# Performance work log

Measured on AMD Instinct MI355X. Metric: run time of the kernel, lower is better.

Reference implementation:

```python
import jax, jax.numpy as jnp
import numpy as np

NB_HEAD = 8
SIZE_PER_HEAD = 64
MAX_LEN = 1024
MASK_PENALTY = 1e12


def setup_inputs() -> dict:
    key = jax.random.key(0)
    ks = jax.random.split(key, 6)
    B, L, D_IN = 8, MAX_LEN, 512
    D_OUT = NB_HEAD * SIZE_PER_HEAD
    return {
        "Q_seq": jax.random.normal(ks[0], (B, L, D_IN), dtype=jnp.float32),
        "K_seq": jax.random.normal(ks[1], (B, L, D_IN), dtype=jnp.float32),
        "V_seq": jax.random.normal(ks[2], (B, L, D_IN), dtype=jnp.float32),
        "WQ": jax.random.normal(ks[3], (D_IN, D_OUT), dtype=jnp.float32) * 0.03,
        "WK": jax.random.normal(ks[4], (D_IN, D_OUT), dtype=jnp.float32) * 0.03,
        "WV": jax.random.normal(ks[5], (D_IN, D_OUT), dtype=jnp.float32) * 0.03,
    }


def reference(Q_seq, K_seq, V_seq, WQ, WK, WV):
    B, L, _ = Q_seq.shape
    H, D = NB_HEAD, SIZE_PER_HEAD
    # project and split heads: [B, L, H*D] -> [B, H, L, D]
    q = (Q_seq @ WQ).reshape(B, L, H, D).transpose(0, 2, 1, 3)
    k = (K_seq @ WK).reshape(B, L, H, D).transpose(0, 2, 1, 3)
    v = (V_seq @ WV).reshape(B, L, H, D).transpose(0, 2, 1, 3)
    scale = 1.0 / jnp.sqrt(jnp.asarray(D, dtype=q.dtype))
    scores = jnp.einsum('bhqd,bhkd->bhqk', q, k) * scale  # [B,H,L,L]
    # Mask(): eye+cumsum construction == causal mask (penalize key > query)
    causal = jnp.triu(jnp.ones((L, L), dtype=scores.dtype), k=1)
    scores = scores - causal * MASK_PENALTY
    A = jax.nn.softmax(scores, axis=-1)
    O = jnp.einsum('bhqk,bhkd->bhqd', A, v)  # [B,H,L,D]
    return O.transpose(0, 2, 1, 3).reshape(B, L, H * D)
```

## Files before the change

kernel.cpp:

```cpp
#include <hip/hip_runtime.h>

#define NH 8
#define DH 64
#define SL 1024
#define NB 8
#define DIN 512
#define DOUT 512
#define PS 72

typedef __bf16 bf16x8 __attribute__((ext_vector_type(8)));
typedef float floatx4 __attribute__((ext_vector_type(4)));
typedef unsigned short ushortx8 __attribute__((ext_vector_type(8)));

__device__ __forceinline__ unsigned short f2bf(float f) {
    unsigned int u = __builtin_bit_cast(unsigned int, f);
    u += 0x7FFFu + ((u >> 16) & 1u);
    return (unsigned short)(u >> 16);
}

__device__ __forceinline__ floatx4 mfma_bf16(bf16x8 a, bf16x8 b, floatx4 c) {
    return __builtin_amdgcn_mfma_f32_16x16x32_bf16(a, b, c, 0, 0, 0);
}

__device__ __forceinline__ void gld_lds16(const unsigned short* g, unsigned short* l) {
    __builtin_amdgcn_global_load_lds(
        (const __attribute__((address_space(1))) unsigned int*)g,
        (__attribute__((address_space(3))) unsigned int*)l, 16, 0, 0);
}

__device__ __forceinline__ unsigned int pack_bf2(float a, float b) {
    return __builtin_amdgcn_perm(__builtin_bit_cast(unsigned int, b),
                                 __builtin_bit_cast(unsigned int, a), 0x07060302u);
}

__global__ __launch_bounds__(256) void xbf_kernel(const float* __restrict__ Qs,
                                                  const float* __restrict__ Ks,
                                                  const float* __restrict__ Vs,
                                                  unsigned short* __restrict__ xb) {
    const int z = blockIdx.y;
    const float* X = (z == 0) ? Qs : (z == 1 ? Ks : Vs);
    const int t = blockIdx.x * 256 + threadIdx.x;
    const int row = t >> 6, c = t & 63;
    const float4 a = *(const float4*)(X + t * 8);
    const float4 b = *(const float4*)(X + t * 8 + 4);
    ushortx8 o;
    o[0] = f2bf(a.x); o[1] = f2bf(a.y); o[2] = f2bf(a.z); o[3] = f2bf(a.w);
    o[4] = f2bf(b.x); o[5] = f2bf(b.y); o[6] = f2bf(b.z); o[7] = f2bf(b.w);
    const int dst = (((row >> 7) * 8 + (c >> 3)) * 128 + (row & 127)) * 64 +
                    (((c & 7) ^ (row & 7)) * 8);
    *(ushortx8*)(xb + z * 8192 * DIN + dst) = o;
}

__global__ __launch_bounds__(256) void wt_kernel(const float* __restrict__ WQ,
                                                 const float* __restrict__ WK,
                                                 const float* __restrict__ WV,
                                                 unsigned short* __restrict__ wt) {
    __shared__ unsigned short tile[64][68];
    const int z = blockIdx.z;
    const float* W = (z == 0) ? WQ : (z == 1 ? WK : WV);
    const int k0 = blockIdx.y * 64, n0 = blockIdx.x * 64;
    const int tn = threadIdx.x & 63, tk = threadIdx.x >> 6;
#pragma unroll
    for (int i = 0; i < 16; ++i) {
        const int kk = tk + i * 4;
        tile[tn][kk] = f2bf(W[(k0 + kk) * DOUT + n0 + tn]);
    }
    __syncthreads();
#pragma unroll
    for (int i = 0; i < 16; ++i) {
        const int nn = tk + i * 4;
        const int n = n0 + nn, k = k0 + tn;
        const int dst = (((z * 4 + (n >> 7)) * 8 + (k >> 6)) * 128 + (n & 127)) * 64 +
                        ((((k >> 3) & 7) ^ (n & 7)) * 8) + (k & 7);
        wt[dst] = tile[nn][tn];
    }
}

__global__ __launch_bounds__(256) void proj_kernel(const unsigned short* __restrict__ xbt,
                                                   const unsigned short* __restrict__ wtt,
                                                   unsigned short* __restrict__ qw,
                                                   unsigned short* __restrict__ ks,
                                                   unsigned short* __restrict__ vs) {
    __shared__ __align__(16) unsigned short S[16384];
    unsigned short* As = S;
    unsigned short* Bs = S + 8192;
    const int z = blockIdx.z;
    const int mblk = blockIdx.x, nblk = blockIdx.y;
    const int w = threadIdx.x >> 6, lane = threadIdx.x & 63;
    const int l15 = lane & 15, quad = lane >> 4;
    const int wm = w >> 1, wn = w & 1;
    const int soff = lane * 8;
    const unsigned short* Ab = xbt + z * (8192 * DIN) + mblk * 8 * 8192 + (w * 4) * 512 + soff;
    const unsigned short* Bb = wtt + (z * 4 + nblk) * 8 * 8192 + (w * 4) * 512 + soff;
    unsigned short* Asw = &As[(w * 4) * 512];
    unsigned short* Bsw = &Bs[(w * 4) * 512];

    floatx4 acc[4][4];
#pragma unroll
    for (int i = 0; i < 4; ++i)
#pragma unroll
        for (int j = 0; j < 4; ++j) acc[i][j] = floatx4{0.f, 0.f, 0.f, 0.f};

    for (int kblk = 0; kblk < 8; ++kblk) {
        __syncthreads();
#pragma unroll
        for (int i = 0; i < 4; ++i) {
            gld_lds16(Ab + kblk * 8192 + i * 512, Asw + i * 512);
            gld_lds16(Bb + kblk * 8192 + i * 512, Bsw + i * 512);
        }
        __syncthreads();
#pragma unroll
        for (int ksub = 0; ksub < 2; ++ksub) {
            bf16x8 af[4], bfr[4];
#pragma unroll
            for (int mi = 0; mi < 4; ++mi) {
                const int row = wm * 64 + mi * 16 + l15;
                af[mi] = *(const bf16x8*)&As[row * 64 + (((quad + ksub * 4) ^ (l15 & 7)) * 8)];
            }
#pragma unroll
            for (int nt = 0; nt < 4; ++nt) {
                const int row = wn * 64 + nt * 16 + l15;
                bfr[nt] = *(const bf16x8*)&Bs[row * 64 + (((quad + ksub * 4) ^ (l15 & 7)) * 8)];
            }
#pragma unroll
            for (int mi = 0; mi < 4; ++mi)
#pragma unroll
                for (int nt = 0; nt < 4; ++nt)
                    acc[mi][nt] = mfma_bf16(af[mi], bfr[nt], acc[mi][nt]);
        }
    }

    __syncthreads();
#pragma unroll
    for (int mi = 0; mi < 4; ++mi)
#pragma unroll
        for (int nt = 0; nt < 4; ++nt)
#pragma unroll
            for (int r = 0; r < 4; ++r) {
                const int a = wm * 64 + mi * 16 + quad * 4 + r;
                const int c = wn * 64 + nt * 16 + l15;
                const int h = c >> 6, dh = c & 63;
                float v = acc[mi][nt][r];
                int lidx;
                if (z == 0) {
                    v *= 0.18033688f;
                    lidx = h * 8192 + a * 64 + dh;
                } else if (z == 1) {
                    lidx = (((((h << 3) + (a >> 4)) << 1) | (dh >> 5))) * 512 +
                           (a & 15) * 32 + (dh & 31);
                } else {
                    const int s64 = ((a & 15) << 2) | ((a >> 4) & 3);
                    lidx = ((((h << 1) | (a >> 6)) << 1) | (s64 >> 5)) * 2048 +
                           dh * 32 + (s64 & 31);
                }
                S[lidx] = f2bf(v);
            }
    __syncthreads();

    const int b = mblk >> 3;
    const int li0 = (mblk & 7) * 128;
    const int tid = threadIdx.x;
    unsigned short* outp = (z == 0) ? qw : (z == 1 ? ks : vs);
#pragma unroll
    for (int j = 0; j < 8; ++j) {
        const int off = j * 2048 + tid * 8;
        const ushortx8 val = *(const ushortx8*)(S + off);
        int gidx;
        if (z == 0) {
            const int h = off >> 13, rem = off & 8191;
            gidx = ((b * 8 + nblk * 2 + h) * 1024 + li0) * 64 + rem;
        } else if (z == 1) {
            const int region = off >> 9, pos = off & 511;
            const int h = region >> 4, g = (region >> 1) & 7, d5 = region & 1;
            gidx = (((b * 8 + nblk * 2 + h) * 64 + (li0 >> 4) + g) * 2 + d5) * 512 + pos;
        } else {
            const int region = off >> 11, pos = off & 2047;
            const int h = region >> 2, l6 = (region >> 1) & 1, s5 = region & 1;
            gidx = ((b * 8 + nblk * 2 + h) * 32 + (li0 >> 5) + l6 * 2 + s5) * 2048 + pos;
        }
        *(ushortx8*)(outp + gidx) = val;
    }
}

__global__ __launch_bounds__(256) void attn_kernel(const unsigned short* __restrict__ qw,
                                                   const unsigned short* __restrict__ ksp,
                                                   const unsigned short* __restrict__ vsp,
                                                   float* __restrict__ out) {
    __shared__ union {
        unsigned short Ps[4][16 * PS];
        float Cb[2][64][21];
    } sh;
    const int w = threadIdx.x >> 6;
    const int lane = threadIdx.x & 63;
    const int l15 = lane & 15, quad = lane >> 4;
    const int bh = blockIdx.y;
    const int b = bh >> 3, h = bh & 7;
    const int tile = (w < 2) ? blockIdx.x : 63 - blockIdx.x;
    const int half = w & 1;
    const int m0 = tile * 16;

    const unsigned short* qp = qw + (bh * SL + m0 + l15) * DH + quad * 8;
    const bf16x8 aQ0 = *(const bf16x8*)qp;
    const bf16x8 aQ1 = *(const bf16x8*)(qp + 32);

    const unsigned short* ksb = ksp + (bh * 64) * 2 * 512 + l15 * 32 + quad * 8;
    const unsigned short* vsb = vsp + (bh * 32 * 64 + l15) * 32 + quad * 8;
    unsigned short* myPs = sh.Ps[w];

    float lrow[4] = {0.f, 0.f, 0.f, 0.f};
    floatx4 o0 = {0.f, 0.f, 0.f, 0.f}, o1 = o0, o2 = o0, o3 = o0;
    const floatx4 zf = {0.f, 0.f, 0.f, 0.f};

    auto TAIL = [&](int kt, floatx4* s, bool domask, const bf16x8* v0, const bf16x8* v1) {
#pragma unroll
        for (int r = 0; r < 4; ++r) {
            const int row = m0 + quad * 4 + r;
            float p[4];
#pragma unroll
            for (int t = 0; t < 4; ++t) {
                float e = __builtin_amdgcn_exp2f(s[t][r]);
                if (domask && (kt + t * 16 + l15 > row)) e = 0.f;
                p[t] = e;
            }
            lrow[r] += (p[0] + p[1]) + (p[2] + p[3]);
            uint2 pk;
            pk.x = pack_bf2(p[0], p[1]);
            pk.y = pack_bf2(p[2], p[3]);
            *(uint2*)(myPs + (quad * 4 + r) * PS + l15 * 4) = pk;
        }
        __builtin_amdgcn_wave_barrier();
        const bf16x8 aP0 = *(const bf16x8*)(myPs + l15 * PS + quad * 8);
        const bf16x8 aP1 = *(const bf16x8*)(myPs + l15 * PS + 32 + quad * 8);
        __builtin_amdgcn_wave_barrier();
        o0 = mfma_bf16(aP1, v1[0], mfma_bf16(aP0, v0[0], o0));
        o1 = mfma_bf16(aP1, v1[1], mfma_bf16(aP0, v0[1], o1));
        o2 = mfma_bf16(aP1, v1[2], mfma_bf16(aP0, v0[2], o2));
        o3 = mfma_bf16(aP1, v1[3], mfma_bf16(aP0, v0[3], o3));
    };

    auto BODY = [&](int kt) {
        const unsigned short* vb = vsb + (kt >> 5) * 2048;
        bf16x8 v0[4], v1[4];
#pragma unroll
        for (int dt = 0; dt < 4; ++dt) {
            v0[dt] = *(const bf16x8*)(vb + dt * 512);
            v1[dt] = *(const bf16x8*)(vb + dt * 512 + 2048);
        }
        const unsigned short* kp = ksb + (kt >> 4) * 1024;
        floatx4 s[4];
#pragma unroll
        for (int t = 0; t < 4; ++t) {
            const bf16x8 k0 = *(const bf16x8*)(kp + t * 1024);
            const bf16x8 k1 = *(const bf16x8*)(kp + t * 1024 + 512);
            s[t] = mfma_bf16(aQ1, k1, mfma_bf16(aQ0, k0, zf));
        }
        TAIL(kt, s, false, v0, v1);
    };

    auto BODYM = [&](int kt) {
        const unsigned short* vb = vsb + (kt >> 5) * 2048;
        bf16x8 v0[4], v1[4];
#pragma unroll
        for (int dt = 0; dt < 4; ++dt) {
            v0[dt] = *(const bf16x8*)(vb + dt * 512);
            v1[dt] = *(const bf16x8*)(vb + dt * 512 + 2048);
        }
        const unsigned short* kp = ksb + (kt >> 4) * 1024;
        floatx4 s[4] = {zf, zf, zf, zf};
#pragma unroll
        for (int t = 0; t < 4; ++t) {
            if (kt + t * 16 <= m0 + 15) {
                const bf16x8 k0 = *(const bf16x8*)(kp + t * 1024);
                const bf16x8 k1 = *(const bf16x8*)(kp + t * 1024 + 512);
                s[t] = mfma_bf16(aQ1, k1, mfma_bf16(aQ0, k0, zf));
            }
        }
        TAIL(kt, s, true, v0, v1);
    };

    const int nf = (tile + 4) >> 2;
    const int last = nf - 1;
    for (int j = half; j < last; j += 2) BODY(j * 64);
    if ((last & 1) == half) BODYM(last * 64);

    __syncthreads();
    if (half == 1) {
        float* cb = &sh.Cb[w >> 1][lane][0];
#pragma unroll
        for (int r = 0; r < 4; ++r) {
            cb[r] = o0[r]; cb[4 + r] = o1[r];
            cb[8 + r] = o2[r]; cb[12 + r] = o3[r];
            cb[16 + r] = lrow[r];
        }
    }
    __syncthreads();
    if (half == 0) {
        const float* cb = &sh.Cb[w >> 1][lane][0];
#pragma unroll
        for (int r = 0; r < 4; ++r) {
            o0[r] += cb[r]; o1[r] += cb[4 + r];
            o2[r] += cb[8 + r]; o3[r] += cb[12 + r];
            lrow[r] += cb[16 + r];
        }
#pragma unroll
        for (int r = 0; r < 4; ++r) {
            float l = lrow[r];
            l += __shfl_xor(l, 1);
            l += __shfl_xor(l, 2);
            l += __shfl_xor(l, 4);
            l += __shfl_xor(l, 8);
            const float inv = 1.0f / l;
            const int row = m0 + quad * 4 + r;
            float* op = out + (b * SL + row) * DOUT + h * DH + l15;
            op[0]  = o0[r] * inv;
            op[16] = o1[r] * inv;
            op[32] = o2[r] * inv;
            op[48] = o3[r] * inv;
        }
    }
}

extern "C" void kernel_launch(void* const* d_in, const int* in_sizes, int n_in,
                              void* d_out, int out_size, void* d_ws, size_t ws_size,
                              hipStream_t stream) {
    const float* Qs = (const float*)d_in[0];
    const float* Ks = (const float*)d_in[1];
    const float* Vs = (const float*)d_in[2];
    const float* WQ = (const float*)d_in[3];
    const float* WK = (const float*)d_in[4];
    const float* WV = (const float*)d_in[5];
    float* out = (float*)d_out;

    unsigned short* xb = (unsigned short*)d_ws;
    unsigned short* wt = xb + 3 * 8192 * DIN;
    unsigned short* qw = wt + 3 * DIN * DOUT;
    unsigned short* ks = qw + NB * NH * SL * DH;
    unsigned short* vs = ks + NB * NH * SL * DH;

    xbf_kernel<<<dim3(8192 * DIN / (256 * 8), 3), 256, 0, stream>>>(Qs, Ks, Vs, xb);
    wt_kernel<<<dim3(DOUT / 64, DIN / 64, 3), 256, 0, stream>>>(WQ, WK, WV, wt);
    proj_kernel<<<dim3(64, 4, 3), 256, 0, stream>>>(xb, wt, qw, ks, vs);
    attn_kernel<<<dim3(32, NB * NH), 256, 0, stream>>>(qw, ks, vs, out);
}
```

Measured before the change: 166.3 us.

## Pre-pack operands in MFMA fragment order and drop LDS staging in projection GEMM

The bf16 conversion kernels now write X and W^T in a layout where each 16-row by 8-column fragment is contiguous, so the projection GEMM loads MFMA operands straight from global memory into registers. This removes the LDS staging with global_load_lds and the two block barriers per k-step. The Q output layout is also changed to fragment order, and the attention kernel's Q loads are updated to match. The cost is that operands are no longer shared through LDS: each wave re-reads A and B tiles from global or L2, which raises memory traffic and exposes load latency without explicit double buffering.

```diff
diff --git a/kernel.cpp b/kernel.cpp
--- a/kernel.cpp
+++ b/kernel.cpp
@@ -22,12 +22,6 @@
     return __builtin_amdgcn_mfma_f32_16x16x32_bf16(a, b, c, 0, 0, 0);
 }
 
-__device__ __forceinline__ void gld_lds16(const unsigned short* g, unsigned short* l) {
-    __builtin_amdgcn_global_load_lds(
-        (const __attribute__((address_space(1))) unsigned int*)g,
-        (__attribute__((address_space(3))) unsigned int*)l, 16, 0, 0);
-}
-
 __device__ __forceinline__ unsigned int pack_bf2(float a, float b) {
     return __builtin_amdgcn_perm(__builtin_bit_cast(unsigned int, b),
                                  __builtin_bit_cast(unsigned int, a), 0x07060302u);
@@ -39,23 +33,27 @@
                                                   unsigned short* __restrict__ xb) {
     const int z = blockIdx.y;
     const float* X = (z == 0) ? Qs : (z == 1 ? Ks : Vs);
-    const int t = blockIdx.x * 256 + threadIdx.x;
-    const int row = t >> 6, c = t & 63;
-    const float4 a = *(const float4*)(X + t * 8);
-    const float4 b = *(const float4*)(X + t * 8 + 4);
-    ushortx8 o;
-    o[0] = f2bf(a.x); o[1] = f2bf(a.y); o[2] = f2bf(a.z); o[3] = f2bf(a.w);
-    o[4] = f2bf(b.x); o[5] = f2bf(b.y); o[6] = f2bf(b.z); o[7] = f2bf(b.w);
-    const int dst = (((row >> 7) * 8 + (c >> 3)) * 128 + (row & 127)) * 64 +
-                    (((c & 7) ^ (row & 7)) * 8);
-    *(ushortx8*)(xb + z * 8192 * DIN + dst) = o;
+    const int u = blockIdx.x * 256 + threadIdx.x;
+    const int c = u & 63;
+    const int row0 = (u >> 6) * 4;
+    ushortx8 ob[4];
+#pragma unroll
+    for (int j = 0; j < 4; ++j) {
+        const float4 a = *(const float4*)(X + (row0 + j) * DIN + c * 8);
+        const float4 b = *(const float4*)(X + (row0 + j) * DIN + c * 8 + 4);
+        ob[j][0] = f2bf(a.x); ob[j][1] = f2bf(a.y); ob[j][2] = f2bf(a.z); ob[j][3] = f2bf(a.w);
+        ob[j][4] = f2bf(b.x); ob[j][5] = f2bf(b.y); ob[j][6] = f2bf(b.z); ob[j][7] = f2bf(b.w);
+    }
+    unsigned short* dst = xb + z * 8192 * DIN + ((row0 >> 4) * 64 + c) * 128 + (row0 & 15) * 8;
+#pragma unroll
+    for (int j = 0; j < 4; ++j) *(ushortx8*)(dst + j * 8) = ob[j];
 }
 
 __global__ __launch_bounds__(256) void wt_kernel(const float* __restrict__ WQ,
                                                  const float* __restrict__ WK,
                                                  const float* __restrict__ WV,
                                                  unsigned short* __restrict__ wt) {
-    __shared__ unsigned short tile[64][68];
+    __shared__ unsigned short tile[64][72];
     const int z = blockIdx.z;
     const float* W = (z == 0) ? WQ : (z == 1 ? WK : WV);
     const int k0 = blockIdx.y * 64, n0 = blockIdx.x * 64;
@@ -66,13 +64,14 @@
         tile[tn][kk] = f2bf(W[(k0 + kk) * DOUT + n0 + tn]);
     }
     __syncthreads();
-#pragma unroll
-    for (int i = 0; i < 16; ++i) {
-        const int nn = tk + i * 4;
-        const int n = n0 + nn, k = k0 + tn;
-        const int dst = (((z * 4 + (n >> 7)) * 8 + (k >> 6)) * 128 + (n & 127)) * 64 +
-                        ((((k >> 3) & 7) ^ (n & 7)) * 8) + (k & 7);
-        wt[dst] = tile[nn][tn];
+    unsigned short* o = wt + z * DIN * DOUT;
+#pragma unroll
+    for (int it = 0; it < 2; ++it) {
+        const int ch = it * 256 + threadIdx.x;
+        const int n_loc = ch >> 3, kc = ch & 7;
+        const ushortx8 v = *(const ushortx8*)&tile[n_loc][kc * 8];
+        const int n = n0 + n_loc, k = k0 + kc * 8;
+        *(ushortx8*)(o + ((n >> 4) * 64 + (k >> 3)) * 128 + (n & 15) * 8) = v;
     }
 }
 
@@ -82,18 +81,14 @@
                                                    unsigned short* __restrict__ ks,
                                                    unsigned short* __restrict__ vs) {
     __shared__ __align__(16) unsigned short S[16384];
-    unsigned short* As = S;
-    unsigned short* Bs = S + 8192;
     const int z = blockIdx.z;
     const int mblk = blockIdx.x, nblk = blockIdx.y;
     const int w = threadIdx.x >> 6, lane = threadIdx.x & 63;
     const int l15 = lane & 15, quad = lane >> 4;
     const int wm = w >> 1, wn = w & 1;
-    const int soff = lane * 8;
-    const unsigned short* Ab = xbt + z * (8192 * DIN) + mblk * 8 * 8192 + (w * 4) * 512 + soff;
-    const unsigned short* Bb = wtt + (z * 4 + nblk) * 8 * 8192 + (w * 4) * 512 + soff;
-    unsigned short* Asw = &As[(w * 4) * 512];
-    unsigned short* Bsw = &Bs[(w * 4) * 512];
+    const int loff = quad * 128 + l15 * 8;
+    const unsigned short* Ab = xbt + z * (8192 * DIN) + (mblk * 8 + wm * 4) * 8192 + loff;
+    const unsigned short* Bb = wtt + z * (DIN * DOUT) + (nblk * 8 + wn * 4) * 8192 + loff;
 
     floatx4 acc[4][4];
 #pragma unroll
@@ -102,35 +97,24 @@
         for (int j = 0; j < 4; ++j) acc[i][j] = floatx4{0.f, 0.f, 0.f, 0.f};
 
     for (int kblk = 0; kblk < 8; ++kblk) {
-        __syncthreads();
-#pragma unroll
-        for (int i = 0; i < 4; ++i) {
-            gld_lds16(Ab + kblk * 8192 + i * 512, Asw + i * 512);
-            gld_lds16(Bb + kblk * 8192 + i * 512, Bsw + i * 512);
-        }
-        __syncthreads();
+        bf16x8 af[2][4], bfr[2][4];
 #pragma unroll
         for (int ksub = 0; ksub < 2; ++ksub) {
-            bf16x8 af[4], bfr[4];
-#pragma unroll
-            for (int mi = 0; mi < 4; ++mi) {
-                const int row = wm * 64 + mi * 16 + l15;
-                af[mi] = *(const bf16x8*)&As[row * 64 + (((quad + ksub * 4) ^ (l15 & 7)) * 8)];
-            }
-#pragma unroll
-            for (int nt = 0; nt < 4; ++nt) {
-                const int row = wn * 64 + nt * 16 + l15;
-                bfr[nt] = *(const bf16x8*)&Bs[row * 64 + (((quad + ksub * 4) ^ (l15 & 7)) * 8)];
-            }
+            const int ko = (kblk * 8 + ksub * 4) * 128;
+#pragma unroll
+            for (int mi = 0; mi < 4; ++mi) af[ksub][mi] = *(const bf16x8*)(Ab + mi * 8192 + ko);
+#pragma unroll
+            for (int nt = 0; nt < 4; ++nt) bfr[ksub][nt] = *(const bf16x8*)(Bb + nt * 8192 + ko);
+        }
+#pragma unroll
+        for (int ksub = 0; ksub < 2; ++ksub)
 #pragma unroll
             for (int mi = 0; mi < 4; ++mi)
 #pragma unroll
                 for (int nt = 0; nt < 4; ++nt)
-                    acc[mi][nt] = mfma_bf16(af[mi], bfr[nt], acc[mi][nt]);
-        }
-    }
-
-    __syncthreads();
+                    acc[mi][nt] = mfma_bf16(af[ksub][mi], bfr[ksub][nt], acc[mi][nt]);
+    }
+
 #pragma unroll
     for (int mi = 0; mi < 4; ++mi)
 #pragma unroll
@@ -144,7 +128,7 @@
                 int lidx;
                 if (z == 0) {
                     v *= 0.18033688f;
-                    lidx = h * 8192 + a * 64 + dh;
+                    lidx = h * 8192 + (a >> 4) * 1024 + (dh >> 3) * 128 + (a & 15) * 8 + (dh & 7);
                 } else if (z == 1) {
                     lidx = (((((h << 3) + (a >> 4)) << 1) | (dh >> 5))) * 512 +
                            (a & 15) * 32 + (dh & 31);
@@ -167,8 +151,8 @@
         const ushortx8 val = *(const ushortx8*)(S + off);
         int gidx;
         if (z == 0) {
-            const int h = off >> 13, rem = off & 8191;
-            gidx = ((b * 8 + nblk * 2 + h) * 1024 + li0) * 64 + rem;
+            const int h = off >> 13, o13 = off & 8191;
+            gidx = ((b * 8 + nblk * 2 + h) * 64 + (li0 >> 4) + (o13 >> 10)) * 1024 + (o13 & 1023);
         } else if (z == 1) {
             const int region = off >> 9, pos = off & 511;
             const int h = region >> 4, g = (region >> 1) & 7, d5 = region & 1;
@@ -199,9 +183,9 @@
     const int half = w & 1;
     const int m0 = tile * 16;
 
-    const unsigned short* qp = qw + (bh * SL + m0 + l15) * DH + quad * 8;
+    const unsigned short* qp = qw + (bh * 64 + tile) * 1024 + quad * 128 + l15 * 8;
     const bf16x8 aQ0 = *(const bf16x8*)qp;
-    const bf16x8 aQ1 = *(const bf16x8*)(qp + 32);
+    const bf16x8 aQ1 = *(const bf16x8*)(qp + 512);
 
     const unsigned short* ksb = ksp + (bh * 64) * 2 * 512 + l15 * 32 + quad * 8;
     const unsigned short* vsb = vsp + (bh * 32 * 64 + l15) * 32 + quad * 8;
@@ -337,7 +321,7 @@
     unsigned short* ks = qw + NB * NH * SL * DH;
     unsigned short* vs = ks + NB * NH * SL * DH;
 
-    xbf_kernel<<<dim3(8192 * DIN / (256 * 8), 3), 256, 0, stream>>>(Qs, Ks, Vs, xb);
+    xbf_kernel<<<dim3(512, 3), 256, 0, stream>>>(Qs, Ks, Vs, xb);
     wt_kernel<<<dim3(DOUT / 64, DIN / 64, 3), 256, 0, stream>>>(WQ, WK, WV, wt);
     proj_kernel<<<dim3(64, 4, 3), 256, 0, stream>>>(xb, wt, qw, ks, vs);
     attn_kernel<<<dim3(32, NB * NH), 256, 0, stream>>>(qw, ks, vs, out);
```

Measured after the change: 187.0 us. +12.4%, slower.
